# Kernel tuning notes

Measured on AMD Instinct MI355X. Metric: run time of the kernel, lower is better.

## Reference

```python
import jax, jax.numpy as jnp
import numpy as np

L_LEVELS = 10
LEVEL_DIM = 4
BASE_RES = 16
T_HASH = 2 ** 21
DEG_VIEW = 4
DENSITY_BIAS = -1.0
RGB_PADDING = 0.001
RES = (BASE_RES * 2 ** np.arange(L_LEVELS)).astype(np.float32)  # 16..8192
CORNERS = np.array([[(i >> 2) & 1, (i >> 1) & 1, i & 1] for i in range(8)], np.int32)  # [8,3]
P1 = jnp.uint32(2654435761)
P2 = jnp.uint32(805459861)


def hash_grid_encode(pts, embeddings):
    """pts [N,3] in [-1,1]; embeddings [L,T,D] -> [N,L,D] trilinear hash-grid features."""
    x01 = (pts + 1.0) * 0.5  # [N,3] in [0,1]

    def level(emb, r):
        pos = x01 * r - 0.5  # align_corners=False style
        p0 = jnp.floor(pos)
        frac = pos - p0  # [N,3]
        coords = (p0.astype(jnp.int32)[:, None, :] + CORNERS).astype(jnp.uint32)  # [N,8,3]
        h = coords[..., 0] ^ (coords[..., 1] * P1) ^ (coords[..., 2] * P2)
        idx = (h & jnp.uint32(T_HASH - 1)).astype(jnp.int32)  # [N,8]
        w = jnp.prod(jnp.where(CORNERS == 1, frac[:, None, :], 1.0 - frac[:, None, :]), axis=-1)  # [N,8]
        vals = emb[idx]  # [N,8,D]
        return jnp.einsum('ncd,nc->nd', vals, w)

    feats = jax.vmap(level)(embeddings, jnp.asarray(RES))  # [L,N,D]
    return jnp.moveaxis(feats, 0, 1)  # [N,L,D]


def pos_enc(d, min_deg=0, max_deg=DEG_VIEW):
    scales = 2.0 ** jnp.arange(min_deg, max_deg, dtype=jnp.float32)
    xb = (d[..., None, :] * scales[:, None]).reshape(*d.shape[:-1], -1)  # [...,3*deg]
    four = jnp.sin(jnp.concatenate([xb, xb + 0.5 * jnp.pi], axis=-1))
    return jnp.concatenate([d, four], axis=-1)  # [..., 3 + 6*deg] = 27


def setup_inputs() -> dict:
    key = jax.random.key(0)
    ks = jax.random.split(key, 10)
    B, S, n = 1024, 32, 6
    means = jax.random.uniform(ks[0], (B, S, n, 3), minval=-1.0, maxval=1.0)
    stds = jax.random.uniform(ks[1], (B, S, n), minval=0.001, maxval=0.05)
    vd = jax.random.normal(ks[2], (B, 3))
    viewdirs = vd / jnp.linalg.norm(vd, axis=-1, keepdims=True)
    embeddings = jax.random.normal(ks[3], (L_LEVELS, T_HASH, LEVEL_DIM)) * 0.1

    def lin(k, i, o):
        return jax.random.normal(k, (i, o)) * (1.0 / np.sqrt(i))

    return {
        'rand': 0,
        'means': means, 'stds': stds, 'viewdirs': viewdirs, 'embeddings': embeddings,
        'Wd0': lin(ks[4], 40, 64), 'bd0': jnp.zeros(64),
        'Wd1': lin(ks[5], 64, 256), 'bd1': jnp.zeros(256),
        'Wv0': lin(ks[6], 283, 256), 'bv0': jnp.zeros(256),
        'Wv1': lin(ks[7], 539, 256), 'bv1': jnp.zeros(256),
        'Wr': lin(ks[8], 256, 3), 'br': jnp.zeros(3),
    }


def reference(rand, means, stds, viewdirs, embeddings, Wd0, bd0, Wd1, bd1,
              Wv0, bv0, Wv1, bv1, Wr, br):
    B, S, n = means.shape[:3]
    # --- predict_density ---
    feats = hash_grid_encode(means.reshape(-1, 3), embeddings)
    feats = feats.reshape(B, S, n, L_LEVELS, LEVEL_DIM)
    gs = jnp.asarray(RES)
    # erf re-weighting by per-level grid size (ZipNeRF anti-aliasing)
    w = jax.lax.erf(1.0 / jnp.clip(jnp.sqrt(8.0 * stds[..., None] ** 2 * gs ** 2), 1e-10))  # [B,S,n,L]
    feat = (feats * w[..., None]).mean(axis=-3).reshape(B, S, L_LEVELS * LEVEL_DIM)  # mean over multisamples n
    h = jax.nn.relu(feat @ Wd0 + bd0)
    x = h @ Wd1 + bd1  # [B,S,256] bottleneck
    density = jax.nn.softplus(x[..., 0] + DENSITY_BIAS)
    # --- view-dependent rgb branch ---
    dir_enc = pos_enc(viewdirs)  # [B,27]
    de = jnp.broadcast_to(dir_enc[:, None, :], (B, S, dir_enc.shape[-1]))
    x_in = jnp.concatenate([x, de], axis=-1)  # [B,S,283]
    h = jax.nn.relu(x_in @ Wv0 + bv0)
    h = jnp.concatenate([h, x_in], axis=-1)  # skip connection at layer 0 -> [B,S,539]
    h = jax.nn.relu(h @ Wv1 + bv1)
    rgb = jax.nn.sigmoid(h @ Wr + br)  # rgb_premultiplier=1, rgb_bias=0
    rgb = rgb * (1.0 + 2.0 * RGB_PADDING) - RGB_PADDING
    return density, rgb
```

## Files before the change

kernel.cpp:

```cpp
#include <hip/hip_runtime.h>

#define HASH_T    2097152u
#define HASH_MASK 2097151u
#define PRIME1 2654435761u
#define PRIME2 805459861u

typedef __attribute__((ext_vector_type(8))) short bf16x8;
typedef __attribute__((ext_vector_type(4))) float f32x4;
typedef __attribute__((ext_vector_type(4))) unsigned short us4;

#define LDS_STRIDE 328

__device__ __forceinline__ unsigned short bf16_hi(float x){
    unsigned u = __float_as_uint(x);
    return (unsigned short)((u + 0x7FFFu + ((u >> 16) & 1u)) >> 16);
}
__device__ __forceinline__ float bf16f(unsigned short h){
    return __uint_as_float((unsigned)h << 16);
}
__device__ __forceinline__ void split2(float x, unsigned short& h, unsigned short& l){
    h = bf16_hi(x);
    l = bf16_hi(x - bf16f(h));
}

__global__ __launch_bounds__(256) void pack_weights_kernel(
    const float* __restrict__ Wd0, const float* __restrict__ Wd1,
    const float* __restrict__ Wv0, const float* __restrict__ Wv1,
    unsigned short* __restrict__ pk)
{
    int tid = blockIdx.x * 256 + threadIdx.x;
    if (tid >= 424 * 512) return;
    int pair = tid >> 9;
    int li   = tid & 511;
    int lane = li >> 3, j = li & 7;
    int kq = ((lane >> 4) << 3) + j;
    int cl = lane & 15;
    float w;
    if (pair < 8) {
        int idx = pair; int kt = idx >> 2, ct = idx & 3;
        int k = kt * 32 + kq, c = ct * 16 + cl;
        w = (k < 40) ? Wd0[k * 64 + c] : 0.0f;
    } else if (pair < 40) {
        int idx = pair - 8; int kt = idx >> 4, ct = idx & 15;
        int k = kt * 32 + kq, c = ct * 16 + cl;
        w = Wd1[k * 256 + c];
    } else if (pair < 168) {
        int idx = pair - 40; int kt = idx >> 4, ct = idx & 15;
        int k = kt * 32 + kq, c = ct * 16 + cl;
        w = Wv0[k * 256 + c];
    } else {
        int idx = pair - 168;
        int kt = idx >> 4, ct = idx & 15;
        int k = kt * 32 + kq, c = ct * 16 + cl;
        int refr = (k < 256) ? (k + 256) : (k - 256);
        w = Wv1[refr * 256 + c];
    }
    unsigned short h, l; split2(w, h, l);
    pk[(size_t)pair * 1024 + li]       = h;
    pk[(size_t)pair * 1024 + 512 + li] = l;
}

template<int KT, int NC>
__device__ __forceinline__ void gemm32(
    const unsigned short* __restrict__ pkBase, int NCT, int ct0, int kOff,
    const unsigned short (*Ahi)[LDS_STRIDE], const unsigned short (*Alo)[LDS_STRIDE],
    int lane, f32x4 acc[NC][2])
{
    const int r = lane & 15;
    const int kg = (lane >> 4) * 8;
    bf16x8 ah[NC], al[NC];
    #pragma unroll
    for (int ci = 0; ci < NC; ++ci) {
        const unsigned short* pf = pkBase + (size_t)(ct0 + ci) * 1024 + (size_t)lane * 8;
        ah[ci] = *reinterpret_cast<const bf16x8*>(pf);
        al[ci] = *reinterpret_cast<const bf16x8*>(pf + 512);
    }
    #pragma unroll
    for (int kt = 0; kt < KT; ++kt) {
        bf16x8 ahn[NC], aln[NC];
        if (kt + 1 < KT) {
            #pragma unroll
            for (int ci = 0; ci < NC; ++ci) {
                const unsigned short* pf = pkBase
                    + (size_t)((kt + 1) * NCT + ct0 + ci) * 1024 + (size_t)lane * 8;
                ahn[ci] = *reinterpret_cast<const bf16x8*>(pf);
                aln[ci] = *reinterpret_cast<const bf16x8*>(pf + 512);
            }
        }
        const int ke = kOff + kt * 32 + kg;
        bf16x8 bh[2], bl[2];
        #pragma unroll
        for (int st = 0; st < 2; ++st) {
            bh[st] = *reinterpret_cast<const bf16x8*>(&Ahi[st * 16 + r][ke]);
            bl[st] = *reinterpret_cast<const bf16x8*>(&Alo[st * 16 + r][ke]);
        }
        #pragma unroll
        for (int ci = 0; ci < NC; ++ci) {
            #pragma unroll
            for (int st = 0; st < 2; ++st) {
                acc[ci][st] = __builtin_amdgcn_mfma_f32_16x16x32_bf16(ah[ci], bh[st], acc[ci][st], 0, 0, 0);
                acc[ci][st] = __builtin_amdgcn_mfma_f32_16x16x32_bf16(ah[ci], bl[st], acc[ci][st], 0, 0, 0);
                acc[ci][st] = __builtin_amdgcn_mfma_f32_16x16x32_bf16(al[ci], bh[st], acc[ci][st], 0, 0, 0);
            }
        }
        if (kt + 1 < KT) {
            #pragma unroll
            for (int ci = 0; ci < NC; ++ci) { ah[ci] = ahn[ci]; al[ci] = aln[ci]; }
        }
    }
}

template<int NC, bool RELU>
__device__ __forceinline__ void epi32(
    f32x4 acc[NC][2], int ct0, int lane, const float* bias, int outOff,
    unsigned short (*Ahi)[LDS_STRIDE], unsigned short (*Alo)[LDS_STRIDE])
{
    const int r = lane & 15, g = lane >> 4;
    #pragma unroll
    for (int ci = 0; ci < NC; ++ci) {
        const int c0 = (ct0 + ci) * 16 + g * 4;
        const float4 bb = *reinterpret_cast<const float4*>(&bias[c0]);
        #pragma unroll
        for (int st = 0; st < 2; ++st) {
            const int s = st * 16 + r;
            float v[4] = { acc[ci][st][0] + bb.x, acc[ci][st][1] + bb.y,
                           acc[ci][st][2] + bb.z, acc[ci][st][3] + bb.w };
            us4 H, L;
            #pragma unroll
            for (int q = 0; q < 4; ++q) {
                float vv = RELU ? fmaxf(v[q], 0.0f) : v[q];
                unsigned short h, l; split2(vv, h, l);
                H[q] = h; L[q] = l;
            }
            *reinterpret_cast<us4*>(&Ahi[s][outOff + c0]) = H;
            *reinterpret_cast<us4*>(&Alo[s][outOff + c0]) = L;
        }
    }
}

__global__ __launch_bounds__(256, 3) void zip_fused_kernel(
    const float* __restrict__ means, const float* __restrict__ stds,
    const float* __restrict__ vdirs, const float* __restrict__ emb,
    const unsigned short* __restrict__ pk,
    const float* __restrict__ bd0, const float* __restrict__ bd1,
    const float* __restrict__ Wv0, const float* __restrict__ bv0,
    const float* __restrict__ Wv1, const float* __restrict__ bv1,
    const float* __restrict__ Wr,  const float* __restrict__ br,
    float* __restrict__ outD, float* __restrict__ outRGB)
{
    __shared__ __align__(16) unsigned short sAhi[32][LDS_STRIDE];
    __shared__ __align__(16) unsigned short sAlo[32][LDS_STRIDE];
    __shared__ float sDe[32];
    __shared__ float sDv0[256];
    __shared__ float sDv1[256];

    const int t = threadIdx.x;
    const int lane = t & 63;
    const int w = t >> 6;
    const int b = blockIdx.x;
    const int base = b * 32;

    if (t < 192) {
        int s = t / 6, j = t - s * 6;
        us4 z = {0, 0, 0, 0};
        *reinterpret_cast<us4*>(&sAhi[s][40 + j * 4]) = z;
        *reinterpret_cast<us4*>(&sAlo[s][40 + j * 4]) = z;
    }
    if (t < 27) {
        float d0 = vdirs[b * 3 + 0], d1 = vdirs[b * 3 + 1], d2 = vdirs[b * 3 + 2];
        float val;
        if (t < 3) val = (t == 0) ? d0 : ((t == 1) ? d1 : d2);
        else {
            int u = t - 3, half = u / 12, jk = u % 12;
            int j = jk / 3, k = jk % 3;
            float dk = (k == 0) ? d0 : ((k == 1) ? d1 : d2);
            float xb = dk * (float)(1 << j);
            val = sinf(half ? (xb + 1.57079632679489662f) : xb);
        }
        sDe[t] = val;
    }
    __syncthreads();

    {
        const int s = t >> 3, n = t & 7;
        const bool act = (n < 6);
        float mx = 0.f, my = 0.f, mz = 0.f, sd2_8 = 0.f;
        if (act) {
            const float* mp = means + ((size_t)(base + s) * 6 + n) * 3;
            mx = mp[0]; my = mp[1]; mz = mp[2];
            float sd = stds[(size_t)(base + s) * 6 + n];
            sd2_8 = 8.0f * sd * sd;
        }
        const float inv6 = 1.0f / 6.0f;
        #pragma unroll 2
        for (int l = 0; l < 10; ++l) {
            float r = (float)(16 << l);
            float a0 = 0.f, a1 = 0.f, a2 = 0.f, a3 = 0.f;
            if (act) {
                float px = (mx + 1.0f) * 0.5f * r - 0.5f;
                float py = (my + 1.0f) * 0.5f * r - 0.5f;
                float pz = (mz + 1.0f) * 0.5f * r - 0.5f;
                float fx = floorf(px), fy = floorf(py), fz = floorf(pz);
                float rx = px - fx, ry = py - fy, rz = pz - fz;
                int ix = (int)fx, iy = (int)fy, iz = (int)fz;
                unsigned hx[2] = { (unsigned)ix,          (unsigned)(ix + 1) };
                unsigned hy[2] = { (unsigned)iy * PRIME1, (unsigned)(iy + 1) * PRIME1 };
                unsigned hz[2] = { (unsigned)iz * PRIME2, (unsigned)(iz + 1) * PRIME2 };
                float wx[2] = { 1.0f - rx, rx };
                float wy[2] = { 1.0f - ry, ry };
                float wz[2] = { 1.0f - rz, rz };
                float wl = erff(1.0f / fmaxf(sqrtf(sd2_8 * r * r), 1e-10f));
                #pragma unroll
                for (int c = 0; c < 8; ++c) {
                    int cx = (c >> 2) & 1, cy = (c >> 1) & 1, cz = c & 1;
                    unsigned idx = (hx[cx] ^ hy[cy] ^ hz[cz]) & HASH_MASK;
                    const float4 e = *reinterpret_cast<const float4*>(
                        emb + ((size_t)l * HASH_T + idx) * 4u);
                    float wgt = wx[cx] * wy[cy] * wz[cz];
                    a0 += wgt * e.x; a1 += wgt * e.y; a2 += wgt * e.z; a3 += wgt * e.w;
                }
                a0 *= wl; a1 *= wl; a2 *= wl; a3 *= wl;
            }
            #pragma unroll
            for (int m = 1; m < 8; m <<= 1) {
                a0 += __shfl_xor(a0, m);
                a1 += __shfl_xor(a1, m);
                a2 += __shfl_xor(a2, m);
                a3 += __shfl_xor(a3, m);
            }
            if (n == 0) {
                float o[4] = { a0 * inv6, a1 * inv6, a2 * inv6, a3 * inv6 };
                us4 H, L;
                #pragma unroll
                for (int q = 0; q < 4; ++q) {
                    unsigned short h, lo; split2(o[q], h, lo);
                    H[q] = h; L[q] = lo;
                }
                *reinterpret_cast<us4*>(&sAhi[s][l * 4]) = H;
                *reinterpret_cast<us4*>(&sAlo[s][l * 4]) = L;
            }
        }
    }
    __syncthreads();

    {
        int c = t;
        float a0 = bv0[c], a1 = bv1[c];
        #pragma unroll 3
        for (int k = 0; k < 27; ++k) {
            float dv = sDe[k];
            a0 += dv * Wv0[(256 + k) * 256 + c];
            a1 += dv * Wv1[(512 + k) * 256 + c];
        }
        sDv0[c] = a0; sDv1[c] = a1;
    }
    __syncthreads();

    {
        f32x4 acc[1][2] = {};
        gemm32<2, 1>(pk, 4, w, 0, sAhi, sAlo, lane, acc);
        __syncthreads();
        epi32<1, true>(acc, w, lane, bd0, 0, sAhi, sAlo);
    }
    __syncthreads();

    {
        f32x4 acc[4][2] = {};
        gemm32<2, 4>(pk + 8192, 16, w * 4, 0, sAhi, sAlo, lane, acc);
        if (w == 0 && (lane >> 4) == 0) {
            #pragma unroll
            for (int st = 0; st < 2; ++st) {
                float x0 = acc[0][st][0] + bd1[0];
                int s = st * 16 + (lane & 15);
                float vv = x0 - 1.0f;
                outD[base + s] = fmaxf(vv, 0.0f) + log1pf(expf(-fabsf(vv)));
            }
        }
        __syncthreads();
        epi32<4, false>(acc, w * 4, lane, bd1, 64, sAhi, sAlo);
    }
    __syncthreads();

    f32x4 px[4][2] = {};
    gemm32<8, 4>(pk + 172032, 16, w * 4, 64, sAhi, sAlo, lane, px);
    __syncthreads();

    {
        f32x4 acc[4][2] = {};
        gemm32<8, 4>(pk + 40960, 16, w * 4, 64, sAhi, sAlo, lane, acc);
        __syncthreads();
        epi32<4, true>(acc, w * 4, lane, sDv0, 64, sAhi, sAlo);
    }
    __syncthreads();

    {
        gemm32<8, 4>(pk + 303104, 16, w * 4, 64, sAhi, sAlo, lane, px);
        __syncthreads();
        epi32<4, true>(px, w * 4, lane, sDv1, 64, sAhi, sAlo);
    }
    __syncthreads();

    {
        int s = t >> 3, j = t & 7, k0 = 64 + j * 32;
        float p0 = 0.f, p1 = 0.f, p2 = 0.f;
        #pragma unroll 2
        for (int q = 0; q < 4; ++q) {
            us4 vh[2], vl[2];
            *reinterpret_cast<uint4*>(vh) = *reinterpret_cast<const uint4*>(&sAhi[s][k0 + q * 8]);
            *reinterpret_cast<uint4*>(vl) = *reinterpret_cast<const uint4*>(&sAlo[s][k0 + q * 8]);
            #pragma unroll
            for (int e = 0; e < 8; ++e) {
                int k = j * 32 + q * 8 + e;
                float hv = bf16f(((const unsigned short*)vh)[e]) + bf16f(((const unsigned short*)vl)[e]);
                p0 += hv * Wr[k * 3 + 0];
                p1 += hv * Wr[k * 3 + 1];
                p2 += hv * Wr[k * 3 + 2];
            }
        }
        #pragma unroll
        for (int m = 1; m < 8; m <<= 1) {
            p0 += __shfl_xor(p0, m);
            p1 += __shfl_xor(p1, m);
            p2 += __shfl_xor(p2, m);
        }
        if (j < 3) {
            float a = ((j == 0) ? p0 : (j == 1) ? p1 : p2) + br[j];
            float sg = 1.0f / (1.0f + expf(-a));
            outRGB[(size_t)(base + s) * 3 + j] = sg * 1.002f - 0.001f;
        }
    }
}

extern "C" void kernel_launch(void* const* d_in, const int* in_sizes, int n_in,
                              void* d_out, int out_size, void* d_ws, size_t ws_size,
                              hipStream_t stream) {
    const float* means = (const float*)d_in[1];
    const float* stds_ = (const float*)d_in[2];
    const float* vdirs = (const float*)d_in[3];
    const float* emb   = (const float*)d_in[4];
    const float* Wd0 = (const float*)d_in[5];
    const float* bd0 = (const float*)d_in[6];
    const float* Wd1 = (const float*)d_in[7];
    const float* bd1 = (const float*)d_in[8];
    const float* Wv0 = (const float*)d_in[9];
    const float* bv0 = (const float*)d_in[10];
    const float* Wv1 = (const float*)d_in[11];
    const float* bv1 = (const float*)d_in[12];
    const float* Wr  = (const float*)d_in[13];
    const float* br  = (const float*)d_in[14];

    const int B  = in_sizes[3] / 3;
    const int NS = B * 32;

    unsigned short* pk = (unsigned short*)d_ws;

    hipLaunchKernelGGL(pack_weights_kernel, dim3((424 * 512 + 255) / 256), dim3(256), 0, stream,
                       Wd0, Wd1, Wv0, Wv1, pk);

    float* outD   = (float*)d_out;
    float* outRGB = outD + NS;
    hipLaunchKernelGGL(zip_fused_kernel, dim3(B), dim3(256), 0, stream,
                       means, stds_, vdirs, emb, pk,
                       bd0, bd1, Wv0, bv0, Wv1, bv1, Wr, br,
                       outD, outRGB);
}
```

Baseline: 191.4 us.

## Warp-specialize fused kernel: gather waves prefetch next tile while MLP waves compute

```diff
diff --git a/kernel.cpp b/kernel.cpp
--- a/kernel.cpp
+++ b/kernel.cpp
@@ -9,7 +9,13 @@
 typedef __attribute__((ext_vector_type(4))) float f32x4;
 typedef __attribute__((ext_vector_type(4))) unsigned short us4;
 
-#define LDS_STRIDE 328
+#define XS 328
+#define FS 48
+
+#define MFMA3(acc, ah, al, bh, bl) \
+    acc = __builtin_amdgcn_mfma_f32_16x16x32_bf16(ah, bh, acc, 0, 0, 0); \
+    acc = __builtin_amdgcn_mfma_f32_16x16x32_bf16(ah, bl, acc, 0, 0, 0); \
+    acc = __builtin_amdgcn_mfma_f32_16x16x32_bf16(al, bh, acc, 0, 0, 0);
 
 __device__ __forceinline__ unsigned short bf16_hi(float x){
     unsigned u = __float_as_uint(x);
@@ -61,9 +67,9 @@
 }
 
 template<int KT, int NC>
-__device__ __forceinline__ void gemm32(
+__device__ __forceinline__ void gemmX(
     const unsigned short* __restrict__ pkBase, int NCT, int ct0, int kOff,
-    const unsigned short (*Ahi)[LDS_STRIDE], const unsigned short (*Alo)[LDS_STRIDE],
+    const unsigned short (*Bhi)[XS], const unsigned short (*Blo)[XS],
     int lane, f32x4 acc[NC][2])
 {
     const int r = lane & 15;
@@ -91,16 +97,14 @@
         bf16x8 bh[2], bl[2];
         #pragma unroll
         for (int st = 0; st < 2; ++st) {
-            bh[st] = *reinterpret_cast<const bf16x8*>(&Ahi[st * 16 + r][ke]);
-            bl[st] = *reinterpret_cast<const bf16x8*>(&Alo[st * 16 + r][ke]);
+            bh[st] = *reinterpret_cast<const bf16x8*>(&Bhi[st * 16 + r][ke]);
+            bl[st] = *reinterpret_cast<const bf16x8*>(&Blo[st * 16 + r][ke]);
         }
         #pragma unroll
         for (int ci = 0; ci < NC; ++ci) {
             #pragma unroll
             for (int st = 0; st < 2; ++st) {
-                acc[ci][st] = __builtin_amdgcn_mfma_f32_16x16x32_bf16(ah[ci], bh[st], acc[ci][st], 0, 0, 0);
-                acc[ci][st] = __builtin_amdgcn_mfma_f32_16x16x32_bf16(ah[ci], bl[st], acc[ci][st], 0, 0, 0);
-                acc[ci][st] = __builtin_amdgcn_mfma_f32_16x16x32_bf16(al[ci], bh[st], acc[ci][st], 0, 0, 0);
+                MFMA3(acc[ci][st], ah[ci], al[ci], bh[st], bl[st]);
             }
         }
         if (kt + 1 < KT) {
@@ -111,9 +115,9 @@
 }
 
 template<int NC, bool RELU>
-__device__ __forceinline__ void epi32(
+__device__ __forceinline__ void epiX(
     f32x4 acc[NC][2], int ct0, int lane, const float* bias, int outOff,
-    unsigned short (*Ahi)[LDS_STRIDE], unsigned short (*Alo)[LDS_STRIDE])
+    unsigned short (*Xhi)[XS], unsigned short (*Xlo)[XS])
 {
     const int r = lane & 15, g = lane >> 4;
     #pragma unroll
@@ -132,13 +136,81 @@
                 unsigned short h, l; split2(vv, h, l);
                 H[q] = h; L[q] = l;
             }
-            *reinterpret_cast<us4*>(&Ahi[s][outOff + c0]) = H;
-            *reinterpret_cast<us4*>(&Alo[s][outOff + c0]) = L;
-        }
-    }
-}
-
-__global__ __launch_bounds__(256, 3) void zip_fused_kernel(
+            *reinterpret_cast<us4*>(&Xhi[s][outOff + c0]) = H;
+            *reinterpret_cast<us4*>(&Xlo[s][outOff + c0]) = L;
+        }
+    }
+}
+
+__device__ __forceinline__ float dircalc(int u, const float* __restrict__ vd)
+{
+    float d0 = vd[0], d1 = vd[1], d2 = vd[2];
+    if (u < 3) return (u == 0) ? d0 : ((u == 1) ? d1 : d2);
+    int v = u - 3, half = v / 12, jk = v % 12;
+    int j = jk / 3, k = jk % 3;
+    float dk = (k == 0) ? d0 : ((k == 1) ? d1 : d2);
+    float xb = dk * (float)(1 << j);
+    return sinf(half ? (xb + 1.57079632679489662f) : xb);
+}
+
+__device__ __forceinline__ void gather2lv(
+    int l0, bool ga, float mx, float my, float mz, float sd28,
+    int lane, int s, const float* __restrict__ emb,
+    unsigned short (*Fhi)[FS], unsigned short (*Flo)[FS])
+{
+    const float inv6 = 1.0f / 6.0f;
+    #pragma unroll
+    for (int dl = 0; dl < 2; ++dl) {
+        const int l = l0 + dl;
+        const float r = (float)(16 << l);
+        float a0 = 0.f, a1 = 0.f, a2 = 0.f, a3 = 0.f;
+        if (ga) {
+            float px = (mx + 1.0f) * 0.5f * r - 0.5f;
+            float py = (my + 1.0f) * 0.5f * r - 0.5f;
+            float pz = (mz + 1.0f) * 0.5f * r - 0.5f;
+            float fx = floorf(px), fy = floorf(py), fz = floorf(pz);
+            float rx = px - fx, ry = py - fy, rz = pz - fz;
+            int ix = (int)fx, iy = (int)fy, iz = (int)fz;
+            unsigned hx[2] = { (unsigned)ix,          (unsigned)(ix + 1) };
+            unsigned hy[2] = { (unsigned)iy * PRIME1, (unsigned)(iy + 1) * PRIME1 };
+            unsigned hz[2] = { (unsigned)iz * PRIME2, (unsigned)(iz + 1) * PRIME2 };
+            float wx[2] = { 1.0f - rx, rx };
+            float wy[2] = { 1.0f - ry, ry };
+            float wz[2] = { 1.0f - rz, rz };
+            float wl = erff(1.0f / fmaxf(sqrtf(sd28 * r * r), 1e-10f));
+            const float* embL = emb + (size_t)l * HASH_T * 4u;
+            #pragma unroll
+            for (int c = 0; c < 8; ++c) {
+                int cx = (c >> 2) & 1, cy = (c >> 1) & 1, cz = c & 1;
+                unsigned idx = (hx[cx] ^ hy[cy] ^ hz[cz]) & HASH_MASK;
+                const float4 e = *reinterpret_cast<const float4*>(embL + (size_t)idx * 4u);
+                float wgt = wx[cx] * wy[cy] * wz[cz];
+                a0 += wgt * e.x; a1 += wgt * e.y; a2 += wgt * e.z; a3 += wgt * e.w;
+            }
+            a0 *= wl; a1 *= wl; a2 *= wl; a3 *= wl;
+        }
+        #pragma unroll
+        for (int m = 1; m < 8; m <<= 1) {
+            a0 += __shfl_xor(a0, m);
+            a1 += __shfl_xor(a1, m);
+            a2 += __shfl_xor(a2, m);
+            a3 += __shfl_xor(a3, m);
+        }
+        if ((lane & 7) == 0) {
+            float o[4] = { a0 * inv6, a1 * inv6, a2 * inv6, a3 * inv6 };
+            us4 H, L;
+            #pragma unroll
+            for (int q = 0; q < 4; ++q) {
+                unsigned short hh, ll; split2(o[q], hh, ll);
+                H[q] = hh; L[q] = ll;
+            }
+            *reinterpret_cast<us4*>(&Fhi[s][l * 4]) = H;
+            *reinterpret_cast<us4*>(&Flo[s][l * 4]) = L;
+        }
+    }
+}
+
+__global__ __launch_bounds__(512, 4) void zip_ws_kernel(
     const float* __restrict__ means, const float* __restrict__ stds,
     const float* __restrict__ vdirs, const float* __restrict__ emb,
     const unsigned short* __restrict__ pk,
@@ -148,186 +220,211 @@
     const float* __restrict__ Wr,  const float* __restrict__ br,
     float* __restrict__ outD, float* __restrict__ outRGB)
 {
-    __shared__ __align__(16) unsigned short sAhi[32][LDS_STRIDE];
-    __shared__ __align__(16) unsigned short sAlo[32][LDS_STRIDE];
-    __shared__ float sDe[32];
-    __shared__ float sDv0[256];
-    __shared__ float sDv1[256];
+    __shared__ __align__(16) unsigned short sFhi[2][32][FS];
+    __shared__ __align__(16) unsigned short sFlo[2][32][FS];
+    __shared__ __align__(16) unsigned short sXhi[32][XS];
+    __shared__ __align__(16) unsigned short sXlo[32][XS];
+    __shared__ float sDe[2][32];
+    __shared__ float sDv0[2][256];
+    __shared__ float sDv1[2][256];
 
     const int t = threadIdx.x;
     const int lane = t & 63;
     const int w = t >> 6;
-    const int b = blockIdx.x;
-    const int base = b * 32;
-
-    if (t < 192) {
-        int s = t / 6, j = t - s * 6;
-        us4 z = {0, 0, 0, 0};
-        *reinterpret_cast<us4*>(&sAhi[s][40 + j * 4]) = z;
-        *reinterpret_cast<us4*>(&sAlo[s][40 + j * 4]) = z;
-    }
-    if (t < 27) {
-        float d0 = vdirs[b * 3 + 0], d1 = vdirs[b * 3 + 1], d2 = vdirs[b * 3 + 2];
-        float val;
-        if (t < 3) val = (t == 0) ? d0 : ((t == 1) ? d1 : d2);
-        else {
-            int u = t - 3, half = u / 12, jk = u % 12;
-            int j = jk / 3, k = jk % 3;
-            float dk = (k == 0) ? d0 : ((k == 1) ? d1 : d2);
-            float xb = dk * (float)(1 << j);
-            val = sinf(half ? (xb + 1.57079632679489662f) : xb);
-        }
-        sDe[t] = val;
-    }
-    __syncthreads();
+    const bool isMlp = (w < 4);
+    const int gt = t & 255;
+    const int gs = gt >> 3, gn = gt & 7;
+    const int tb = blockIdx.x * 2;
 
     {
-        const int s = t >> 3, n = t & 7;
-        const bool act = (n < 6);
-        float mx = 0.f, my = 0.f, mz = 0.f, sd2_8 = 0.f;
-        if (act) {
-            const float* mp = means + ((size_t)(base + s) * 6 + n) * 3;
-            mx = mp[0]; my = mp[1]; mz = mp[2];
-            float sd = stds[(size_t)(base + s) * 6 + n];
-            sd2_8 = 8.0f * sd * sd;
-        }
-        const float inv6 = 1.0f / 6.0f;
-        #pragma unroll 2
-        for (int l = 0; l < 10; ++l) {
-            float r = (float)(16 << l);
-            float a0 = 0.f, a1 = 0.f, a2 = 0.f, a3 = 0.f;
-            if (act) {
-                float px = (mx + 1.0f) * 0.5f * r - 0.5f;
-                float py = (my + 1.0f) * 0.5f * r - 0.5f;
-                float pz = (mz + 1.0f) * 0.5f * r - 0.5f;
-                float fx = floorf(px), fy = floorf(py), fz = floorf(pz);
-                float rx = px - fx, ry = py - fy, rz = pz - fz;
-                int ix = (int)fx, iy = (int)fy, iz = (int)fz;
-                unsigned hx[2] = { (unsigned)ix,          (unsigned)(ix + 1) };
-                unsigned hy[2] = { (unsigned)iy * PRIME1, (unsigned)(iy + 1) * PRIME1 };
-                unsigned hz[2] = { (unsigned)iz * PRIME2, (unsigned)(iz + 1) * PRIME2 };
-                float wx[2] = { 1.0f - rx, rx };
-                float wy[2] = { 1.0f - ry, ry };
-                float wz[2] = { 1.0f - rz, rz };
-                float wl = erff(1.0f / fmaxf(sqrtf(sd2_8 * r * r), 1e-10f));
+        float mx = 0.f, my = 0.f, mz = 0.f, sd28 = 0.f; bool ga = false;
+        if (!isMlp) {
+            ga = (gn < 6);
+            if (ga) {
+                const float* mp = means + ((size_t)(tb * 32 + gs) * 6 + gn) * 3;
+                mx = mp[0]; my = mp[1]; mz = mp[2];
+                float sd = stds[(size_t)(tb * 32 + gs) * 6 + gn];
+                sd28 = 8.0f * sd * sd;
+            }
+            if (gt < 27) sDe[0][gt] = dircalc(gt, vdirs + (size_t)tb * 3);
+        }
+        __syncthreads();
+        if (!isMlp) {
+            #pragma unroll 1
+            for (int lp = 0; lp < 5; ++lp)
+                gather2lv(2 * lp, ga, mx, my, mz, sd28, lane, gs, emb, sFhi[0], sFlo[0]);
+            float a0 = bv0[gt], a1 = bv1[gt];
+            #pragma unroll 3
+            for (int k = 0; k < 27; ++k) {
+                float dv = sDe[0][k];
+                a0 += dv * Wv0[(256 + k) * 256 + gt];
+                a1 += dv * Wv1[(512 + k) * 256 + gt];
+            }
+            sDv0[0][gt] = a0; sDv1[0][gt] = a1;
+        }
+        __syncthreads();
+    }
+
+    #pragma unroll 1
+    for (int it = 0; it < 2; ++it) {
+        const int fb = it;
+        const int nb = fb ^ 1;
+        const int cbase = (tb + it) * 32;
+        const bool gact = (!isMlp) && (it == 0);
+
+        float gmx = 0.f, gmy = 0.f, gmz = 0.f, gsd = 0.f; bool ga = false;
+        if (gact) {
+            ga = (gn < 6);
+            if (ga) {
+                const float* mp = means + ((size_t)((tb + 1) * 32 + gs) * 6 + gn) * 3;
+                gmx = mp[0]; gmy = mp[1]; gmz = mp[2];
+                float sd = stds[(size_t)((tb + 1) * 32 + gs) * 6 + gn];
+                gsd = 8.0f * sd * sd;
+            }
+            if (gt < 27) sDe[nb][gt] = dircalc(gt, vdirs + (size_t)(tb + 1) * 3);
+        }
+
+        f32x4 px[4][2] = {};
+
+        if (isMlp) {
+            f32x4 acc[2] = {};
+            const int r = lane & 15, kg = (lane >> 4) * 8;
+            {
+                const unsigned short* pf = pk + (size_t)w * 1024 + (size_t)lane * 8;
+                bf16x8 ah = *reinterpret_cast<const bf16x8*>(pf);
+                bf16x8 al = *reinterpret_cast<const bf16x8*>(pf + 512);
                 #pragma unroll
-                for (int c = 0; c < 8; ++c) {
-                    int cx = (c >> 2) & 1, cy = (c >> 1) & 1, cz = c & 1;
-                    unsigned idx = (hx[cx] ^ hy[cy] ^ hz[cz]) & HASH_MASK;
-                    const float4 e = *reinterpret_cast<const float4*>(
-                        emb + ((size_t)l * HASH_T + idx) * 4u);
-                    float wgt = wx[cx] * wy[cy] * wz[cz];
-                    a0 += wgt * e.x; a1 += wgt * e.y; a2 += wgt * e.z; a3 += wgt * e.w;
+                for (int st = 0; st < 2; ++st) {
+                    bf16x8 bh = *reinterpret_cast<const bf16x8*>(&sFhi[fb][st * 16 + r][kg]);
+                    bf16x8 bl = *reinterpret_cast<const bf16x8*>(&sFlo[fb][st * 16 + r][kg]);
+                    MFMA3(acc[st], ah, al, bh, bl);
                 }
-                a0 *= wl; a1 *= wl; a2 *= wl; a3 *= wl;
-            }
-            #pragma unroll
-            for (int m = 1; m < 8; m <<= 1) {
-                a0 += __shfl_xor(a0, m);
-                a1 += __shfl_xor(a1, m);
-                a2 += __shfl_xor(a2, m);
-                a3 += __shfl_xor(a3, m);
-            }
-            if (n == 0) {
-                float o[4] = { a0 * inv6, a1 * inv6, a2 * inv6, a3 * inv6 };
+            }
+            {
+                const unsigned short* pf = pk + (size_t)(4 + w) * 1024 + (size_t)lane * 8;
+                bf16x8 ah = *reinterpret_cast<const bf16x8*>(pf);
+                bf16x8 al = *reinterpret_cast<const bf16x8*>(pf + 512);
+                #pragma unroll
+                for (int st = 0; st < 2; ++st) {
+                    bf16x8 bh = {}, bl = {};
+                    if (kg == 0) {
+                        bh = *reinterpret_cast<const bf16x8*>(&sFhi[fb][st * 16 + r][32]);
+                        bl = *reinterpret_cast<const bf16x8*>(&sFlo[fb][st * 16 + r][32]);
+                    }
+                    MFMA3(acc[st], ah, al, bh, bl);
+                }
+            }
+            const int g = lane >> 4;
+            const int c0 = w * 16 + g * 4;
+            const float4 bb = *reinterpret_cast<const float4*>(&bd0[c0]);
+            #pragma unroll
+            for (int st = 0; st < 2; ++st) {
+                const int s = st * 16 + r;
+                float v[4] = { acc[st][0] + bb.x, acc[st][1] + bb.y,
+                               acc[st][2] + bb.z, acc[st][3] + bb.w };
                 us4 H, L;
                 #pragma unroll
                 for (int q = 0; q < 4; ++q) {
-                    unsigned short h, lo; split2(o[q], h, lo);
-                    H[q] = h; L[q] = lo;
+                    unsigned short hh, ll; split2(fmaxf(v[q], 0.0f), hh, ll);
+                    H[q] = hh; L[q] = ll;
                 }
-                *reinterpret_cast<us4*>(&sAhi[s][l * 4]) = H;
-                *reinterpret_cast<us4*>(&sAlo[s][l * 4]) = L;
-            }
-        }
-    }
-    __syncthreads();
-
-    {
-        int c = t;
-        float a0 = bv0[c], a1 = bv1[c];
-        #pragma unroll 3
-        for (int k = 0; k < 27; ++k) {
-            float dv = sDe[k];
-            a0 += dv * Wv0[(256 + k) * 256 + c];
-            a1 += dv * Wv1[(512 + k) * 256 + c];
-        }
-        sDv0[c] = a0; sDv1[c] = a1;
-    }
-    __syncthreads();
-
-    {
-        f32x4 acc[1][2] = {};
-        gemm32<2, 1>(pk, 4, w, 0, sAhi, sAlo, lane, acc);
-        __syncthreads();
-        epi32<1, true>(acc, w, lane, bd0, 0, sAhi, sAlo);
-    }
-    __syncthreads();
-
-    {
-        f32x4 acc[4][2] = {};
-        gemm32<2, 4>(pk + 8192, 16, w * 4, 0, sAhi, sAlo, lane, acc);
-        if (w == 0 && (lane >> 4) == 0) {
-            #pragma unroll
-            for (int st = 0; st < 2; ++st) {
-                float x0 = acc[0][st][0] + bd1[0];
-                int s = st * 16 + (lane & 15);
-                float vv = x0 - 1.0f;
-                outD[base + s] = fmaxf(vv, 0.0f) + log1pf(expf(-fabsf(vv)));
-            }
-        }
-        __syncthreads();
-        epi32<4, false>(acc, w * 4, lane, bd1, 64, sAhi, sAlo);
-    }
-    __syncthreads();
-
-    f32x4 px[4][2] = {};
-    gemm32<8, 4>(pk + 172032, 16, w * 4, 64, sAhi, sAlo, lane, px);
-    __syncthreads();
-
-    {
-        f32x4 acc[4][2] = {};
-        gemm32<8, 4>(pk + 40960, 16, w * 4, 64, sAhi, sAlo, lane, acc);
-        __syncthreads();
-        epi32<4, true>(acc, w * 4, lane, sDv0, 64, sAhi, sAlo);
-    }
-    __syncthreads();
-
-    {
-        gemm32<8, 4>(pk + 303104, 16, w * 4, 64, sAhi, sAlo, lane, px);
-        __syncthreads();
-        epi32<4, true>(px, w * 4, lane, sDv1, 64, sAhi, sAlo);
-    }
-    __syncthreads();
-
-    {
-        int s = t >> 3, j = t & 7, k0 = 64 + j * 32;
-        float p0 = 0.f, p1 = 0.f, p2 = 0.f;
-        #pragma unroll 2
-        for (int q = 0; q < 4; ++q) {
-            us4 vh[2], vl[2];
-            *reinterpret_cast<uint4*>(vh) = *reinterpret_cast<const uint4*>(&sAhi[s][k0 + q * 8]);
-            *reinterpret_cast<uint4*>(vl) = *reinterpret_cast<const uint4*>(&sAlo[s][k0 + q * 8]);
-            #pragma unroll
-            for (int e = 0; e < 8; ++e) {
-                int k = j * 32 + q * 8 + e;
-                float hv = bf16f(((const unsigned short*)vh)[e]) + bf16f(((const unsigned short*)vl)[e]);
-                p0 += hv * Wr[k * 3 + 0];
-                p1 += hv * Wr[k * 3 + 1];
-                p2 += hv * Wr[k * 3 + 2];
-            }
-        }
-        #pragma unroll
-        for (int m = 1; m < 8; m <<= 1) {
-            p0 += __shfl_xor(p0, m);
-            p1 += __shfl_xor(p1, m);
-            p2 += __shfl_xor(p2, m);
-        }
-        if (j < 3) {
-            float a = ((j == 0) ? p0 : (j == 1) ? p1 : p2) + br[j];
-            float sg = 1.0f / (1.0f + expf(-a));
-            outRGB[(size_t)(base + s) * 3 + j] = sg * 1.002f - 0.001f;
-        }
+                *reinterpret_cast<us4*>(&sXhi[s][c0]) = H;
+                *reinterpret_cast<us4*>(&sXlo[s][c0]) = L;
+            }
+        } else if (gact) {
+            gather2lv(0, ga, gmx, gmy, gmz, gsd, lane, gs, emb, sFhi[nb], sFlo[nb]);
+        }
+        __syncthreads();
+
+        if (isMlp) {
+            f32x4 acc[4][2] = {};
+            gemmX<2, 4>(pk + 8192, 16, w * 4, 0, sXhi, sXlo, lane, acc);
+            if (w == 0 && (lane >> 4) == 0) {
+                #pragma unroll
+                for (int st = 0; st < 2; ++st) {
+                    float x0 = acc[0][st][0] + bd1[0];
+                    int s = st * 16 + (lane & 15);
+                    float vv = x0 - 1.0f;
+                    outD[cbase + s] = fmaxf(vv, 0.0f) + log1pf(expf(-fabsf(vv)));
+                }
+            }
+            epiX<4, false>(acc, w * 4, lane, bd1, 64, sXhi, sXlo);
+        } else if (gact) {
+            gather2lv(2, ga, gmx, gmy, gmz, gsd, lane, gs, emb, sFhi[nb], sFlo[nb]);
+        }
+        __syncthreads();
+
+        if (isMlp) {
+            gemmX<8, 4>(pk + 172032, 16, w * 4, 64, sXhi, sXlo, lane, px);
+        } else if (gact) {
+            gather2lv(4, ga, gmx, gmy, gmz, gsd, lane, gs, emb, sFhi[nb], sFlo[nb]);
+        }
+        __syncthreads();
+
+        f32x4 h2a[4][2] = {};
+        if (isMlp) {
+            gemmX<8, 4>(pk + 40960, 16, w * 4, 64, sXhi, sXlo, lane, h2a);
+        } else if (gact) {
+            gather2lv(6, ga, gmx, gmy, gmz, gsd, lane, gs, emb, sFhi[nb], sFlo[nb]);
+        }
+        __syncthreads();
+
+        if (isMlp) {
+            epiX<4, true>(h2a, w * 4, lane, sDv0[fb], 64, sXhi, sXlo);
+        } else if (gact) {
+            gather2lv(8, ga, gmx, gmy, gmz, gsd, lane, gs, emb, sFhi[nb], sFlo[nb]);
+        }
+        __syncthreads();
+
+        if (isMlp) {
+            gemmX<8, 4>(pk + 303104, 16, w * 4, 64, sXhi, sXlo, lane, px);
+        } else if (gact) {
+            float a0 = bv0[gt], a1 = bv1[gt];
+            #pragma unroll 3
+            for (int k = 0; k < 27; ++k) {
+                float dv = sDe[nb][k];
+                a0 += dv * Wv0[(256 + k) * 256 + gt];
+                a1 += dv * Wv1[(512 + k) * 256 + gt];
+            }
+            sDv0[nb][gt] = a0; sDv1[nb][gt] = a1;
+        }
+        __syncthreads();
+
+        if (isMlp) {
+            epiX<4, true>(px, w * 4, lane, sDv1[fb], 64, sXhi, sXlo);
+        }
+        __syncthreads();
+
+        if (isMlp) {
+            int s = t >> 3, j = t & 7, k0 = 64 + j * 32;
+            float p0 = 0.f, p1 = 0.f, p2 = 0.f;
+            #pragma unroll 2
+            for (int q = 0; q < 4; ++q) {
+                us4 vh[2], vl[2];
+                *reinterpret_cast<uint4*>(vh) = *reinterpret_cast<const uint4*>(&sXhi[s][k0 + q * 8]);
+                *reinterpret_cast<uint4*>(vl) = *reinterpret_cast<const uint4*>(&sXlo[s][k0 + q * 8]);
+                #pragma unroll
+                for (int e = 0; e < 8; ++e) {
+                    int k = j * 32 + q * 8 + e;
+                    float hv = bf16f(((const unsigned short*)vh)[e]) + bf16f(((const unsigned short*)vl)[e]);
+                    p0 += hv * Wr[k * 3 + 0];
+                    p1 += hv * Wr[k * 3 + 1];
+                    p2 += hv * Wr[k * 3 + 2];
+                }
+            }
+            #pragma unroll
+            for (int m = 1; m < 8; m <<= 1) {
+                p0 += __shfl_xor(p0, m);
+                p1 += __shfl_xor(p1, m);
+                p2 += __shfl_xor(p2, m);
+            }
+            if (j < 3) {
+                float a = ((j == 0) ? p0 : (j == 1) ? p1 : p2) + br[j];
+                float sg = 1.0f / (1.0f + expf(-a));
+                outRGB[(size_t)(cbase + s) * 3 + j] = sg * 1.002f - 0.001f;
+            }
+        }
+        __syncthreads();
     }
 }
 
@@ -359,7 +456,7 @@
 
     float* outD   = (float*)d_out;
     float* outRGB = outD + NS;
-    hipLaunchKernelGGL(zip_fused_kernel, dim3(B), dim3(256), 0, stream,
+    hipLaunchKernelGGL(zip_ws_kernel, dim3(B / 2), dim3(512), 0, stream,
                        means, stds_, vdirs, emb, pk,
                        bd0, bd1, Wv0, bv0, Wv1, bv1, Wr, br,
                        outD, outRGB);
```

Result: slower. 542.4 us (+183.3%).
